# Performance work log

Hardware: AMD Instinct MI355X
Metric: run time of the kernel (lower is better)

The kernel has to match this reference:

```python
import jax, jax.numpy as jnp
import numpy as np

H = 16          # num_heads
D = 1024        # in_features
NH = D // H     # per-head dim
EPS = 1e-5


def _ln(x, g, b):
    m = jnp.mean(x, axis=-1, keepdims=True)
    v = jnp.mean((x - m) ** 2, axis=-1, keepdims=True)
    return (x - m) / jnp.sqrt(v + EPS) * g + b


def _mha(q, k, v, Wq, bq, Wk, bk, Wv, bv, causal):
    # q: [Tq,B,D], k/v: [Tk,B,D]
    Tq, B, _ = q.shape
    Tk = k.shape[0]
    qh = (q @ Wq + bq).reshape(Tq, B, H, NH)
    kh = (k @ Wk + bk).reshape(Tk, B, H, NH)
    vh = (v @ Wv + bv).reshape(Tk, B, H, NH)
    scale = 1.0 / np.float32(np.sqrt(NH))
    logits = jnp.einsum('qbhd,kbhd->bhqk', qh, kh) * scale  # [B,H,Tq,Tk]
    if causal:
        mask = jnp.tril(jnp.ones((Tq, Tk), dtype=bool))
        logits = jnp.where(mask, logits, -jnp.inf)  # softmax over prefix [0..t]
    w = jax.nn.softmax(logits, axis=-1)
    out = jnp.einsum('bhqk,kbhd->qbhd', w, vh).reshape(Tq, B, D)
    return out


def setup_inputs() -> dict:
    key = jax.random.key(0)
    ks = jax.random.split(key, 12)
    s = 0.02
    T, B = 1024, 8
    inp = {
        'encoder_input': jax.random.normal(ks[0], (T, B, D), jnp.float32),
        'decoder_input': jax.random.normal(ks[1], (T, B, D), jnp.float32),
        # self-attention projections
        'Wq1': jax.random.normal(ks[2], (D, D), jnp.float32) * s,
        'bq1': jnp.zeros((D,), jnp.float32),
        'Wk1': jax.random.normal(ks[3], (D, D), jnp.float32) * s,
        'bk1': jnp.zeros((D,), jnp.float32),
        'Wv1': jax.random.normal(ks[4], (D, D), jnp.float32) * s,
        'bv1': jnp.zeros((D,), jnp.float32),
        # cross-attention projections
        'Wq2': jax.random.normal(ks[5], (D, D), jnp.float32) * s,
        'bq2': jnp.zeros((D,), jnp.float32),
        'Wk2': jax.random.normal(ks[6], (D, D), jnp.float32) * s,
        'bk2': jnp.zeros((D,), jnp.float32),
        'Wv2': jax.random.normal(ks[7], (D, D), jnp.float32) * s,
        'bv2': jnp.zeros((D,), jnp.float32),
        # position-wise linear
        'Wl': jax.random.normal(ks[8], (D, D), jnp.float32) * s,
        'bl': jnp.zeros((D,), jnp.float32),
        # layernorms
        'g1': jnp.ones((D,), jnp.float32), 'be1': jnp.zeros((D,), jnp.float32),
        'g2': jnp.ones((D,), jnp.float32), 'be2': jnp.zeros((D,), jnp.float32),
        'g3': jnp.ones((D,), jnp.float32), 'be3': jnp.zeros((D,), jnp.float32),
    }
    return inp


def reference(encoder_input, decoder_input,
              Wq1, bq1, Wk1, bk1, Wv1, bv1,
              Wq2, bq2, Wk2, bk2, Wv2, bv2,
              Wl, bl, g1, be1, g2, be2, g3, be3):
    # causal self-attention (prefix [:t+1] per step == causal mask)
    x = _mha(decoder_input, decoder_input, decoder_input,
             Wq1, bq1, Wk1, bk1, Wv1, bv1, causal=True)
    x = _ln(x + decoder_input, g1, be1)
    # cross-attention over full encoder input
    y = _mha(x, encoder_input, encoder_input,
             Wq2, bq2, Wk2, bk2, Wv2, bv2, causal=False)
    y = _ln(y + x, g2, be2)
    # position-wise linear (no activation in source) + residual + LN
    z = y @ Wl + bl
    out = _ln(z + y, g3, be3)
    return out
```

## Files before the change

kernel.cpp:

```cpp
#include <hip/hip_runtime.h>
#include <hip/hip_bf16.h>

typedef __bf16 bf16x8 __attribute__((ext_vector_type(8)));
typedef float f32x4 __attribute__((ext_vector_type(4)));

#define MFMA16(A, B, C) __builtin_amdgcn_mfma_f32_16x16x32_bf16(A, B, C, 0, 0, 0)

#define GLDS(gp, lp)                                                              \
    __builtin_amdgcn_global_load_lds(                                             \
        (const __attribute__((address_space(1))) void*)(gp),                      \
        (__attribute__((address_space(3))) void*)(lp), 16, 0, 0)

struct PtrW { const float* p[7]; };
__global__ __launch_bounds__(256) void wt_transpose(PtrW W, __hip_bfloat16* __restrict__ Wt) {
    const float* __restrict__ src = W.p[blockIdx.z];
    __hip_bfloat16* __restrict__ dst = Wt + ((size_t)blockIdx.z << 20);
    __shared__ float tile[32][33];
    const int bn = blockIdx.x * 32;
    const int bk = blockIdx.y * 32;
    const int tx = threadIdx.x, ty = threadIdx.y;
#pragma unroll
    for (int i = 0; i < 4; i++) {
        tile[ty + i * 8][tx] = src[(size_t)(bk + ty + i * 8) * 1024 + bn + tx];
    }
    __syncthreads();
#pragma unroll
    for (int i = 0; i < 4; i++) {
        dst[(size_t)(bn + ty + i * 8) * 1024 + bk + tx] =
            __float2bfloat16(tile[tx][ty + i * 8]);
    }
}

struct PtrC { const float* s[2]; __hip_bfloat16* d[2]; };
__global__ __launch_bounds__(256) void to_bf16(PtrC c) {
    const int z = blockIdx.y;
    const int i = (blockIdx.x * 256 + threadIdx.x) * 4;
    const float4 v = *(const float4*)(c.s[z] + i);
    __align__(8) __hip_bfloat16 t[4] = {__float2bfloat16(v.x), __float2bfloat16(v.y),
                                        __float2bfloat16(v.z), __float2bfloat16(v.w)};
    *(uint2*)(c.d[z] + i) = *(const uint2*)t;
}

struct Ptr5 { const float* p[5]; };
__global__ __launch_bounds__(256) void bias_concat(Ptr5 srcs, float* __restrict__ dst) {
    const int i = threadIdx.x * 4;
    *(float4*)(dst + blockIdx.x * 1024 + i) = *(const float4*)(srcs.p[blockIdx.x] + i);
}

__global__ __launch_bounds__(256) void v_transpose(const __hip_bfloat16* __restrict__ src,
                                                   __hip_bfloat16* __restrict__ Vt,
                                                   int S, int coloff) {
    __shared__ __hip_bfloat16 tile[64][72];
    const int t0 = blockIdx.x * 64;
    const int bh = blockIdx.y;
    const int b = bh & 7, h = bh >> 3;
    const int tid = threadIdx.x;
    const int r = tid >> 2, c = (tid & 3) * 16;
    const __hip_bfloat16* sp =
        src + (size_t)((t0 + r) * 8 + b) * S + coloff + h * 64 + c;
    *(uint4*)(&tile[r][c]) = *(const uint4*)(sp);
    *(uint4*)(&tile[r][c + 8]) = *(const uint4*)(sp + 8);
    __syncthreads();
    const int d = tid >> 2, tc = (tid & 3) * 16;
    __align__(16) __hip_bfloat16 tmp[16];
#pragma unroll
    for (int j = 0; j < 16; j++) tmp[j] = tile[tc + j][d];
    __hip_bfloat16* op = Vt + ((size_t)(b * 16 + h) << 16) + (size_t)d * 1024 + t0 + tc;
    *(uint4*)(op) = *(const uint4*)(tmp);
    *(uint4*)(op + 8) = *(const uint4*)(tmp + 8);
}

__global__ __launch_bounds__(256) void gemm_bias_kernel(
    const __hip_bfloat16* __restrict__ A, const __hip_bfloat16* __restrict__ Bt,
    const float* __restrict__ bias, float* __restrict__ Cf,
    __hip_bfloat16* __restrict__ Cb, int M, int N, int K) {
    __shared__ __align__(16) __hip_bfloat16 As[128 * 64];
    __shared__ __align__(16) __hip_bfloat16 Bs[128 * 64];
    const int tid = threadIdx.x;
    const int wave = tid >> 6, lane = tid & 63;
    const int quad = lane >> 4, l16 = lane & 15;
    const int m0 = blockIdx.x * 128, n0 = blockIdx.y * 128;
    const int wm = (wave & 1) * 64, wn = (wave >> 1) * 64;
    const int lrow = lane >> 3;
    const int lch = (lane & 7) ^ (lrow & 7);
    const int sw = l16 & 7;
    const __hip_bfloat16* ap[4];
    const __hip_bfloat16* bp[4];
    __hip_bfloat16* al[4];
    __hip_bfloat16* bl[4];
#pragma unroll
    for (int u = 0; u < 4; u++) {
        const int q = wave * 4 + u;
        const int row = q * 8 + lrow;
        ap[u] = A + (size_t)(m0 + row) * K + lch * 8;
        bp[u] = Bt + (size_t)(n0 + row) * K + lch * 8;
        al[u] = &As[q * 512];
        bl[u] = &Bs[q * 512];
    }
    f32x4 acc[4][4] = {};
    for (int k0 = 0; k0 < K; k0 += 64) {
#pragma unroll
        for (int u = 0; u < 4; u++) {
            GLDS(ap[u] + k0, al[u]);
            GLDS(bp[u] + k0, bl[u]);
        }
        __syncthreads();
        bf16x8 af[2][4], bfr[2][4];
#pragma unroll
        for (int h2 = 0; h2 < 2; h2++)
#pragma unroll
            for (int i = 0; i < 4; i++) {
                af[h2][i] = *(const bf16x8*)(&As[(wm + i * 16 + l16) * 64 +
                                                 (((h2 * 4 + quad) ^ sw) << 3)]);
                bfr[h2][i] = *(const bf16x8*)(&Bs[(wn + i * 16 + l16) * 64 +
                                                  (((h2 * 4 + quad) ^ sw) << 3)]);
            }
        __syncthreads();
#pragma unroll
        for (int h2 = 0; h2 < 2; h2++)
#pragma unroll
            for (int i = 0; i < 4; i++)
#pragma unroll
                for (int j = 0; j < 4; j++)
                    acc[i][j] = MFMA16(af[h2][i], bfr[h2][j], acc[i][j]);
    }
#pragma unroll
    for (int i = 0; i < 4; i++) {
#pragma unroll
        for (int j = 0; j < 4; j++) {
            const int mr = m0 + wm + i * 16 + quad * 4;
            const int nc = n0 + wn + j * 16 + l16;
            const float bv = bias[nc];
#pragma unroll
            for (int r = 0; r < 4; r++) {
                const float v = acc[i][j][r] + bv;
                const size_t idx = (size_t)(mr + r) * N + nc;
                if (Cf) Cf[idx] = v;
                if (Cb) Cb[idx] = __float2bfloat16(v);
            }
        }
    }
}

__global__ __launch_bounds__(256) void attn_kernel(
    const __hip_bfloat16* __restrict__ Qp, const __hip_bfloat16* __restrict__ Kp,
    const __hip_bfloat16* __restrict__ Vt, __hip_bfloat16* __restrict__ Ob,
    int T, int qRS, int kRS, int causal) {
    __shared__ __align__(16) __hip_bfloat16 Ks[64 * 64];
    __shared__ __align__(16) __hip_bfloat16 Vs[64 * 64];
    __shared__ __align__(16) __hip_bfloat16 Ps[4][16 * 64];
    const int tid = threadIdx.x, wave = tid >> 6, lane = tid & 63;
    const int quad = lane >> 4, l16 = lane & 15;
    const int bh = blockIdx.y, b = bh & 7, h = bh >> 3;
    const int q0 = blockIdx.x * 64;
    const int qstride = 8 * qRS, kstride = 8 * kRS;
    const int sw = l16 & 7;
    const float SCL = 0.18033688f;

    const int myq = q0 + wave * 16 + l16;
    bf16x8 qf0, qf1;
    {
        const __hip_bfloat16* qptr = Qp + (size_t)b * qRS + h * 64 + (size_t)myq * qstride;
        qf0 = *(const bf16x8*)(qptr + quad * 8);
        qf1 = *(const bf16x8*)(qptr + 32 + quad * 8);
    }
    const int jk = wave * 2;
    const int lrow = lane >> 3;
    const int lch = (lane & 7) ^ (lrow & 7);
    const __hip_bfloat16* kp0 =
        Kp + (size_t)b * kRS + h * 64 + (size_t)(jk * 8 + lrow) * kstride + lch * 8;
    const __hip_bfloat16* kp1 = kp0 + (size_t)8 * kstride;
    const __hip_bfloat16* vp0 =
        Vt + ((size_t)(b * 16 + h) << 16) + (size_t)(jk * 8 + lrow) * 1024 + lch * 8;
    const __hip_bfloat16* vp1 = vp0 + 8 * 1024;
    __hip_bfloat16* kl0 = &Ks[jk * 512];
    __hip_bfloat16* kl1 = &Ks[jk * 512 + 512];
    __hip_bfloat16* vl0 = &Vs[jk * 512];
    __hip_bfloat16* vl1 = &Vs[jk * 512 + 512];

    float m_i = -1e30f, l_i = 0.f;
    f32x4 o[4] = {};
    const int kend = causal ? (q0 + 64) : T;
    for (int k0 = 0; k0 < kend; k0 += 64) {
        __syncthreads();
        GLDS(kp0 + (size_t)k0 * kstride, kl0);
        GLDS(kp1 + (size_t)k0 * kstride, kl1);
        GLDS(vp0 + k0, vl0);
        GLDS(vp1 + k0, vl1);
        __syncthreads();
        f32x4 s[4];
#pragma unroll
        for (int n = 0; n < 4; n++) {
            f32x4 z = {};
            const int row = (n * 16 + l16) * 64;
            const bf16x8 kf0 = *(const bf16x8*)(&Ks[row + ((quad ^ sw) << 3)]);
            const bf16x8 kf1 = *(const bf16x8*)(&Ks[row + (((quad + 4) ^ sw) << 3)]);
            z = MFMA16(kf0, qf0, z);
            z = MFMA16(kf1, qf1, z);
            s[n] = z;
        }
        const bool nm = causal && (k0 + 63 > q0 + wave * 16);
        float mx = -1e30f;
#pragma unroll
        for (int n = 0; n < 4; n++) {
#pragma unroll
            for (int r = 0; r < 4; r++) {
                float sv = s[n][r] * SCL;
                if (nm && (k0 + n * 16 + quad * 4 + r > myq)) sv = -1e30f;
                s[n][r] = sv;
                mx = fmaxf(mx, sv);
            }
        }
        mx = fmaxf(mx, __shfl_xor(mx, 16));
        mx = fmaxf(mx, __shfl_xor(mx, 32));
        const float mnew = fmaxf(m_i, mx);
        const float alpha = exp2f(m_i - mnew);
        m_i = mnew;
        float sum = 0.f;
#pragma unroll
        for (int n = 0; n < 4; n++) {
            __align__(8) __hip_bfloat16 pb[4];
#pragma unroll
            for (int r = 0; r < 4; r++) {
                const float pv = exp2f(s[n][r] - m_i);
                sum += pv;
                pb[r] = __float2bfloat16(pv);
            }
            const int gcp = 2 * n + (quad >> 1);
            *(uint2*)(&Ps[wave][l16 * 64 + ((gcp ^ sw) << 3) + (quad & 1) * 4]) =
                *(const uint2*)pb;
        }
        sum += __shfl_xor(sum, 16);
        sum += __shfl_xor(sum, 32);
        l_i = l_i * alpha + sum;
#pragma unroll
        for (int mm = 0; mm < 4; mm++) o[mm] = o[mm] * alpha;
        const bf16x8 pf0 = *(const bf16x8*)(&Ps[wave][l16 * 64 + ((quad ^ sw) << 3)]);
        const bf16x8 pf1 =
            *(const bf16x8*)(&Ps[wave][l16 * 64 + (((quad + 4) ^ sw) << 3)]);
#pragma unroll
        for (int mm = 0; mm < 4; mm++) {
            const int vrow = (mm * 16 + l16) * 64;
            const bf16x8 vf0 = *(const bf16x8*)(&Vs[vrow + ((quad ^ sw) << 3)]);
            const bf16x8 vf1 = *(const bf16x8*)(&Vs[vrow + (((quad + 4) ^ sw) << 3)]);
            o[mm] = MFMA16(vf0, pf0, o[mm]);
            o[mm] = MFMA16(vf1, pf1, o[mm]);
        }
    }
    const float inv = 1.0f / l_i;
    __hip_bfloat16* ob = Ob + (size_t)b * 1024 + h * 64 + (size_t)myq * 8192;
#pragma unroll
    for (int mm = 0; mm < 4; mm++) {
        __align__(8) __hip_bfloat16 t[4] = {
            __float2bfloat16(o[mm][0] * inv), __float2bfloat16(o[mm][1] * inv),
            __float2bfloat16(o[mm][2] * inv), __float2bfloat16(o[mm][3] * inv)};
        *(uint2*)(ob + mm * 16 + quad * 4) = *(const uint2*)t;
    }
}

__global__ __launch_bounds__(256) void ln_res_kernel(
    const __hip_bfloat16* __restrict__ a, const float* __restrict__ bres,
    const float* __restrict__ g, const float* __restrict__ be,
    float* __restrict__ outf, __hip_bfloat16* __restrict__ outb) {
    const int row = blockIdx.x;
    const int tid = threadIdx.x;
    const size_t off = (size_t)row * 1024 + tid * 4;
    uint2 ar = *(const uint2*)(a + off);
    const __hip_bfloat16* ah = (const __hip_bfloat16*)&ar;
    const float4 vb = *(const float4*)(bres + off);
    float x0 = __bfloat162float(ah[0]) + vb.x;
    float x1 = __bfloat162float(ah[1]) + vb.y;
    float x2 = __bfloat162float(ah[2]) + vb.z;
    float x3 = __bfloat162float(ah[3]) + vb.w;
    float s = x0 + x1 + x2 + x3;
    float ss = x0 * x0 + x1 * x1 + x2 * x2 + x3 * x3;
#pragma unroll
    for (int w = 32; w >= 1; w >>= 1) {
        s += __shfl_xor(s, w);
        ss += __shfl_xor(ss, w);
    }
    __shared__ float sm[4], sv[4];
    const int wave = tid >> 6;
    if ((tid & 63) == 0) { sm[wave] = s; sv[wave] = ss; }
    __syncthreads();
    s = sm[0] + sm[1] + sm[2] + sm[3];
    ss = sv[0] + sv[1] + sv[2] + sv[3];
    const float mean = s * (1.f / 1024.f);
    const float inv = rsqrtf(ss * (1.f / 1024.f) - mean * mean + 1e-5f);
    const float4 gg = *(const float4*)(g + tid * 4);
    const float4 bb = *(const float4*)(be + tid * 4);
    const float y0 = (x0 - mean) * inv * gg.x + bb.x;
    const float y1 = (x1 - mean) * inv * gg.y + bb.y;
    const float y2 = (x2 - mean) * inv * gg.z + bb.z;
    const float y3 = (x3 - mean) * inv * gg.w + bb.w;
    if (outf) *(float4*)(outf + off) = make_float4(y0, y1, y2, y3);
    if (outb) {
        __align__(8) __hip_bfloat16 t[4] = {__float2bfloat16(y0), __float2bfloat16(y1),
                                            __float2bfloat16(y2), __float2bfloat16(y3)};
        *(uint2*)(outb + off) = *(const uint2*)t;
    }
}

extern "C" void kernel_launch(void* const* d_in, const int* in_sizes, int n_in,
                              void* d_out, int out_size, void* d_ws, size_t ws_size,
                              hipStream_t stream) {
    const float* enc = (const float*)d_in[0];
    const float* dec = (const float*)d_in[1];
    const float* Wq1 = (const float*)d_in[2];
    const float* bq1 = (const float*)d_in[3];
    const float* Wk1 = (const float*)d_in[4];
    const float* bk1 = (const float*)d_in[5];
    const float* Wv1 = (const float*)d_in[6];
    const float* bv1 = (const float*)d_in[7];
    const float* Wq2 = (const float*)d_in[8];
    const float* bq2 = (const float*)d_in[9];
    const float* Wk2 = (const float*)d_in[10];
    const float* bk2 = (const float*)d_in[11];
    const float* Wv2 = (const float*)d_in[12];
    const float* bv2 = (const float*)d_in[13];
    const float* Wl = (const float*)d_in[14];
    const float* bl = (const float*)d_in[15];
    const float* g1 = (const float*)d_in[16];
    const float* be1 = (const float*)d_in[17];
    const float* g2 = (const float*)d_in[18];
    const float* be2 = (const float*)d_in[19];
    const float* g3 = (const float*)d_in[20];
    const float* be3 = (const float*)d_in[21];
    float* outp = (float*)d_out;

    char* p = (char*)d_ws;
    auto alloc = [&](size_t n) {
        char* r = p;
        p += (n + 255) & ~(size_t)255;
        return r;
    };
    const size_t MD = (size_t)8192 * 1024;
    __hip_bfloat16* enc_b = (__hip_bfloat16*)alloc(MD * 2);
    __hip_bfloat16* dec_b = (__hip_bfloat16*)alloc(MD * 2);
    __hip_bfloat16* Wt = (__hip_bfloat16*)alloc((size_t)7 * 1024 * 1024 * 2);
    float* bcat = (float*)alloc((3072 + 2048) * sizeof(float));
    __hip_bfloat16* qkv = (__hip_bfloat16*)alloc(MD * 3 * 2);
    __hip_bfloat16* qb = (__hip_bfloat16*)alloc(MD * 2);
    __hip_bfloat16* attnb = (__hip_bfloat16*)alloc(MD * 2);
    __hip_bfloat16* Vtb = (__hip_bfloat16*)alloc(MD * 2);
    float* xf = (float*)alloc(MD * 4);
    float* yf = (float*)alloc(MD * 4);
    __hip_bfloat16* xb = dec_b;
    __hip_bfloat16* yb = enc_b;

    PtrW wptrs = {{Wq1, Wk1, Wv1, Wq2, Wk2, Wv2, Wl}};
    wt_transpose<<<dim3(32, 32, 7), dim3(32, 8), 0, stream>>>(wptrs, Wt);
    PtrC cp = {{enc, dec}, {enc_b, dec_b}};
    to_bf16<<<dim3(8192, 2), 256, 0, stream>>>(cp);
    Ptr5 bp = {{bq1, bk1, bv1, bk2, bv2}};
    bias_concat<<<5, 256, 0, stream>>>(bp, bcat);

    gemm_bias_kernel<<<dim3(64, 24), 256, 0, stream>>>(dec_b, Wt, bcat, nullptr, qkv,
                                                       8192, 3072, 1024);
    v_transpose<<<dim3(16, 128), 256, 0, stream>>>(qkv, Vtb, 3072, 2048);
    attn_kernel<<<dim3(16, 128), 256, 0, stream>>>(qkv, qkv + 1024, Vtb, attnb,
                                                   1024, 3072, 3072, 1);
    ln_res_kernel<<<8192, 256, 0, stream>>>(attnb, dec, g1, be1, xf, xb);

    gemm_bias_kernel<<<dim3(64, 8), 256, 0, stream>>>(
        xb, Wt + (size_t)3 * 1024 * 1024, bq2, nullptr, qb, 8192, 1024, 1024);
    gemm_bias_kernel<<<dim3(64, 16), 256, 0, stream>>>(
        enc_b, Wt + (size_t)4 * 1024 * 1024, bcat + 3072, nullptr, qkv, 8192, 2048, 1024);
    v_transpose<<<dim3(16, 128), 256, 0, stream>>>(qkv, Vtb, 2048, 1024);
    attn_kernel<<<dim3(16, 128), 256, 0, stream>>>(qb, qkv, Vtb, attnb,
                                                   1024, 1024, 2048, 0);
    ln_res_kernel<<<8192, 256, 0, stream>>>(attnb, xf, g2, be2, yf, yb);

    gemm_bias_kernel<<<dim3(64, 8), 256, 0, stream>>>(
        yb, Wt + (size_t)6 * 1024 * 1024, bl, nullptr, qb, 8192, 1024, 1024);
    ln_res_kernel<<<8192, 256, 0, stream>>>(qb, yf, g3, be3, outp, nullptr);
}
```

Measured before the change: 576.7 us.

## Double-buffer GEMM and attention loads, fold softmax scale into Q projection

```diff
diff --git a/kernel.cpp b/kernel.cpp
--- a/kernel.cpp
+++ b/kernel.cpp
@@ -73,56 +73,57 @@
 __global__ __launch_bounds__(256) void gemm_bias_kernel(
     const __hip_bfloat16* __restrict__ A, const __hip_bfloat16* __restrict__ Bt,
     const float* __restrict__ bias, float* __restrict__ Cf,
-    __hip_bfloat16* __restrict__ Cb, int M, int N, int K) {
-    __shared__ __align__(16) __hip_bfloat16 As[128 * 64];
-    __shared__ __align__(16) __hip_bfloat16 Bs[128 * 64];
+    __hip_bfloat16* __restrict__ Cb, int M, int N, int K,
+    float qscale, int qcols) {
+    __shared__ __align__(16) __hip_bfloat16 As[2][128 * 32];
+    __shared__ __align__(16) __hip_bfloat16 Bs[2][128 * 32];
     const int tid = threadIdx.x;
     const int wave = tid >> 6, lane = tid & 63;
     const int quad = lane >> 4, l16 = lane & 15;
     const int m0 = blockIdx.x * 128, n0 = blockIdx.y * 128;
     const int wm = (wave & 1) * 64, wn = (wave >> 1) * 64;
-    const int lrow = lane >> 3;
-    const int lch = (lane & 7) ^ (lrow & 7);
-    const int sw = l16 & 7;
-    const __hip_bfloat16* ap[4];
-    const __hip_bfloat16* bp[4];
-    __hip_bfloat16* al[4];
-    __hip_bfloat16* bl[4];
-#pragma unroll
-    for (int u = 0; u < 4; u++) {
-        const int q = wave * 4 + u;
-        const int row = q * 8 + lrow;
-        ap[u] = A + (size_t)(m0 + row) * K + lch * 8;
-        bp[u] = Bt + (size_t)(n0 + row) * K + lch * 8;
-        al[u] = &As[q * 512];
-        bl[u] = &Bs[q * 512];
-    }
+    const int srow = lane >> 2;
+    const int lc = (lane & 3) ^ ((lane >> 3) & 3);
+    const __hip_bfloat16* ap[2];
+    const __hip_bfloat16* bp[2];
+    int loff[2];
+#pragma unroll
+    for (int u = 0; u < 2; u++) {
+        const int g = wave * 2 + u;
+        const int row = g * 16 + srow;
+        ap[u] = A + (size_t)(m0 + row) * K + lc * 8;
+        bp[u] = Bt + (size_t)(n0 + row) * K + lc * 8;
+        loff[u] = g * 512;
+    }
+    const int pch = quad ^ ((l16 >> 1) & 3);
     f32x4 acc[4][4] = {};
-    for (int k0 = 0; k0 < K; k0 += 64) {
-#pragma unroll
-        for (int u = 0; u < 4; u++) {
-            GLDS(ap[u] + k0, al[u]);
-            GLDS(bp[u] + k0, bl[u]);
+#pragma unroll
+    for (int u = 0; u < 2; u++) {
+        GLDS(ap[u], &As[0][loff[u]]);
+        GLDS(bp[u], &Bs[0][loff[u]]);
+    }
+    int sel = 0;
+    for (int k0 = 0; k0 < K; k0 += 32) {
+        __syncthreads();
+        if (k0 + 32 < K) {
+#pragma unroll
+            for (int u = 0; u < 2; u++) {
+                GLDS(ap[u] + k0 + 32, &As[sel ^ 1][loff[u]]);
+                GLDS(bp[u] + k0 + 32, &Bs[sel ^ 1][loff[u]]);
+            }
         }
-        __syncthreads();
-        bf16x8 af[2][4], bfr[2][4];
-#pragma unroll
-        for (int h2 = 0; h2 < 2; h2++)
-#pragma unroll
-            for (int i = 0; i < 4; i++) {
-                af[h2][i] = *(const bf16x8*)(&As[(wm + i * 16 + l16) * 64 +
-                                                 (((h2 * 4 + quad) ^ sw) << 3)]);
-                bfr[h2][i] = *(const bf16x8*)(&Bs[(wn + i * 16 + l16) * 64 +
-                                                  (((h2 * 4 + quad) ^ sw) << 3)]);
-            }
-        __syncthreads();
-#pragma unroll
-        for (int h2 = 0; h2 < 2; h2++)
-#pragma unroll
-            for (int i = 0; i < 4; i++)
-#pragma unroll
-                for (int j = 0; j < 4; j++)
-                    acc[i][j] = MFMA16(af[h2][i], bfr[h2][j], acc[i][j]);
+        bf16x8 af[4], bfr[4];
+#pragma unroll
+        for (int i = 0; i < 4; i++) {
+            af[i] = *(const bf16x8*)(&As[sel][(wm + i * 16 + l16) * 32 + pch * 8]);
+            bfr[i] = *(const bf16x8*)(&Bs[sel][(wn + i * 16 + l16) * 32 + pch * 8]);
+        }
+#pragma unroll
+        for (int i = 0; i < 4; i++)
+#pragma unroll
+            for (int j = 0; j < 4; j++)
+                acc[i][j] = MFMA16(af[i], bfr[j], acc[i][j]);
+        sel ^= 1;
     }
 #pragma unroll
     for (int i = 0; i < 4; i++) {
@@ -130,10 +131,11 @@
         for (int j = 0; j < 4; j++) {
             const int mr = m0 + wm + i * 16 + quad * 4;
             const int nc = n0 + wn + j * 16 + l16;
+            const float sc = (nc < qcols) ? qscale : 1.0f;
             const float bv = bias[nc];
 #pragma unroll
             for (int r = 0; r < 4; r++) {
-                const float v = acc[i][j][r] + bv;
+                const float v = (acc[i][j][r] + bv) * sc;
                 const size_t idx = (size_t)(mr + r) * N + nc;
                 if (Cf) Cf[idx] = v;
                 if (Cb) Cb[idx] = __float2bfloat16(v);
@@ -146,16 +148,18 @@
     const __hip_bfloat16* __restrict__ Qp, const __hip_bfloat16* __restrict__ Kp,
     const __hip_bfloat16* __restrict__ Vt, __hip_bfloat16* __restrict__ Ob,
     int T, int qRS, int kRS, int causal) {
-    __shared__ __align__(16) __hip_bfloat16 Ks[64 * 64];
-    __shared__ __align__(16) __hip_bfloat16 Vs[64 * 64];
+    __shared__ __align__(16) __hip_bfloat16 Ks[2][64 * 64];
+    __shared__ __align__(16) __hip_bfloat16 Vs[2][64 * 64];
     __shared__ __align__(16) __hip_bfloat16 Ps[4][16 * 64];
     const int tid = threadIdx.x, wave = tid >> 6, lane = tid & 63;
     const int quad = lane >> 4, l16 = lane & 15;
-    const int bh = blockIdx.y, b = bh & 7, h = bh >> 3;
-    const int q0 = blockIdx.x * 64;
+    const int gid = blockIdx.x;
+    const int bh = (gid & 7) * 16 + (gid >> 7);
+    const int qt = (gid >> 3) & 15;
+    const int b = bh & 7, h = bh >> 3;
+    const int q0 = qt * 64;
     const int qstride = 8 * qRS, kstride = 8 * kRS;
     const int sw = l16 & 7;
-    const float SCL = 0.18033688f;
 
     const int myq = q0 + wave * 16 + l16;
     bf16x8 qf0, qf1;
@@ -164,6 +168,10 @@
         qf0 = *(const bf16x8*)(qptr + quad * 8);
         qf1 = *(const bf16x8*)(qptr + 32 + quad * 8);
     }
+    bf16x8 onesf;
+#pragma unroll
+    for (int i = 0; i < 8; i++) onesf[i] = (__bf16)1.0f;
+
     const int jk = wave * 2;
     const int lrow = lane >> 3;
     const int lch = (lane & 7) ^ (lrow & 7);
@@ -173,81 +181,101 @@
     const __hip_bfloat16* vp0 =
         Vt + ((size_t)(b * 16 + h) << 16) + (size_t)(jk * 8 + lrow) * 1024 + lch * 8;
     const __hip_bfloat16* vp1 = vp0 + 8 * 1024;
-    __hip_bfloat16* kl0 = &Ks[jk * 512];
-    __hip_bfloat16* kl1 = &Ks[jk * 512 + 512];
-    __hip_bfloat16* vl0 = &Vs[jk * 512];
-    __hip_bfloat16* vl1 = &Vs[jk * 512 + 512];
-
-    float m_i = -1e30f, l_i = 0.f;
+    const size_t kinc = (size_t)64 * kstride;
+
+    float m_i = -1e30f;
     f32x4 o[4] = {};
+    f32x4 ol = {};
     const int kend = causal ? (q0 + 64) : T;
+    const int qmax_w = q0 + wave * 16 + 15;
+
+    GLDS(kp0, &Ks[0][jk * 512]);
+    GLDS(kp1, &Ks[0][jk * 512 + 512]);
+    GLDS(vp0, &Vs[0][jk * 512]);
+    GLDS(vp1, &Vs[0][jk * 512 + 512]);
+    const __hip_bfloat16* kn0 = kp0 + kinc;
+    const __hip_bfloat16* kn1 = kp1 + kinc;
+    const __hip_bfloat16* vn0 = vp0 + 64;
+    const __hip_bfloat16* vn1 = vp1 + 64;
+    int sel = 0;
     for (int k0 = 0; k0 < kend; k0 += 64) {
         __syncthreads();
-        GLDS(kp0 + (size_t)k0 * kstride, kl0);
-        GLDS(kp1 + (size_t)k0 * kstride, kl1);
-        GLDS(vp0 + k0, vl0);
-        GLDS(vp1 + k0, vl1);
-        __syncthreads();
-        f32x4 s[4];
-#pragma unroll
-        for (int n = 0; n < 4; n++) {
-            f32x4 z = {};
-            const int row = (n * 16 + l16) * 64;
-            const bf16x8 kf0 = *(const bf16x8*)(&Ks[row + ((quad ^ sw) << 3)]);
-            const bf16x8 kf1 = *(const bf16x8*)(&Ks[row + (((quad + 4) ^ sw) << 3)]);
-            z = MFMA16(kf0, qf0, z);
-            z = MFMA16(kf1, qf1, z);
-            s[n] = z;
+        if (k0 + 64 < kend) {
+            GLDS(kn0, &Ks[sel ^ 1][jk * 512]);
+            GLDS(kn1, &Ks[sel ^ 1][jk * 512 + 512]);
+            GLDS(vn0, &Vs[sel ^ 1][jk * 512]);
+            GLDS(vn1, &Vs[sel ^ 1][jk * 512 + 512]);
+            kn0 += kinc; kn1 += kinc; vn0 += 64; vn1 += 64;
         }
-        const bool nm = causal && (k0 + 63 > q0 + wave * 16);
-        float mx = -1e30f;
-#pragma unroll
-        for (int n = 0; n < 4; n++) {
-#pragma unroll
-            for (int r = 0; r < 4; r++) {
-                float sv = s[n][r] * SCL;
-                if (nm && (k0 + n * 16 + quad * 4 + r > myq)) sv = -1e30f;
-                s[n][r] = sv;
-                mx = fmaxf(mx, sv);
-            }
+        if (!causal || k0 <= qmax_w) {
+            f32x4 s[4];
+#pragma unroll
+            for (int n = 0; n < 4; n++) {
+                f32x4 z = {};
+                const int row = (n * 16 + l16) * 64;
+                const bf16x8 kf0 = *(const bf16x8*)(&Ks[sel][row + ((quad ^ sw) << 3)]);
+                const bf16x8 kf1 =
+                    *(const bf16x8*)(&Ks[sel][row + (((quad + 4) ^ sw) << 3)]);
+                z = MFMA16(kf0, qf0, z);
+                z = MFMA16(kf1, qf1, z);
+                s[n] = z;
+            }
+            const bool nm = causal && (k0 + 63 > q0 + wave * 16);
+            float mx = -1e30f;
+            if (nm) {
+#pragma unroll
+                for (int n = 0; n < 4; n++)
+#pragma unroll
+                    for (int r = 0; r < 4; r++) {
+                        if (k0 + n * 16 + quad * 4 + r > myq) s[n][r] = -1e30f;
+                        mx = fmaxf(mx, s[n][r]);
+                    }
+            } else {
+#pragma unroll
+                for (int n = 0; n < 4; n++)
+#pragma unroll
+                    for (int r = 0; r < 4; r++) mx = fmaxf(mx, s[n][r]);
+            }
+            mx = fmaxf(mx, __shfl_xor(mx, 16));
+            mx = fmaxf(mx, __shfl_xor(mx, 32));
+            const float mnew = fmaxf(m_i, mx);
+            const float alpha = exp2f(m_i - mnew);
+            m_i = mnew;
+#pragma unroll
+            for (int n = 0; n < 4; n++) {
+                const float p0 = exp2f(s[n][0] - m_i);
+                const float p1 = exp2f(s[n][1] - m_i);
+                const float p2 = exp2f(s[n][2] - m_i);
+                const float p3 = exp2f(s[n][3] - m_i);
+                const __hip_bfloat162 pa = __float22bfloat162_rn(make_float2(p0, p1));
+                const __hip_bfloat162 pb = __float22bfloat162_rn(make_float2(p2, p3));
+                uint2 w;
+                w.x = *(const unsigned int*)&pa;
+                w.y = *(const unsigned int*)&pb;
+                const int gcp = 2 * n + (quad >> 1);
+                *(uint2*)(&Ps[wave][l16 * 64 + ((gcp ^ sw) << 3) + (quad & 1) * 4]) = w;
+            }
+#pragma unroll
+            for (int mm = 0; mm < 4; mm++) o[mm] = o[mm] * alpha;
+            ol = ol * alpha;
+            const bf16x8 pf0 = *(const bf16x8*)(&Ps[wave][l16 * 64 + ((quad ^ sw) << 3)]);
+            const bf16x8 pf1 =
+                *(const bf16x8*)(&Ps[wave][l16 * 64 + (((quad + 4) ^ sw) << 3)]);
+#pragma unroll
+            for (int mm = 0; mm < 4; mm++) {
+                const int vrow = (mm * 16 + l16) * 64;
+                const bf16x8 vf0 = *(const bf16x8*)(&Vs[sel][vrow + ((quad ^ sw) << 3)]);
+                const bf16x8 vf1 =
+                    *(const bf16x8*)(&Vs[sel][vrow + (((quad + 4) ^ sw) << 3)]);
+                o[mm] = MFMA16(vf0, pf0, o[mm]);
+                o[mm] = MFMA16(vf1, pf1, o[mm]);
+            }
+            ol = MFMA16(onesf, pf0, ol);
+            ol = MFMA16(onesf, pf1, ol);
         }
-        mx = fmaxf(mx, __shfl_xor(mx, 16));
-        mx = fmaxf(mx, __shfl_xor(mx, 32));
-        const float mnew = fmaxf(m_i, mx);
-        const float alpha = exp2f(m_i - mnew);
-        m_i = mnew;
-        float sum = 0.f;
-#pragma unroll
-        for (int n = 0; n < 4; n++) {
-            __align__(8) __hip_bfloat16 pb[4];
-#pragma unroll
-            for (int r = 0; r < 4; r++) {
-                const float pv = exp2f(s[n][r] - m_i);
-                sum += pv;
-                pb[r] = __float2bfloat16(pv);
-            }
-            const int gcp = 2 * n + (quad >> 1);
-            *(uint2*)(&Ps[wave][l16 * 64 + ((gcp ^ sw) << 3) + (quad & 1) * 4]) =
-                *(const uint2*)pb;
-        }
-        sum += __shfl_xor(sum, 16);
-        sum += __shfl_xor(sum, 32);
-        l_i = l_i * alpha + sum;
-#pragma unroll
-        for (int mm = 0; mm < 4; mm++) o[mm] = o[mm] * alpha;
-        const bf16x8 pf0 = *(const bf16x8*)(&Ps[wave][l16 * 64 + ((quad ^ sw) << 3)]);
-        const bf16x8 pf1 =
-            *(const bf16x8*)(&Ps[wave][l16 * 64 + (((quad + 4) ^ sw) << 3)]);
-#pragma unroll
-        for (int mm = 0; mm < 4; mm++) {
-            const int vrow = (mm * 16 + l16) * 64;
-            const bf16x8 vf0 = *(const bf16x8*)(&Vs[vrow + ((quad ^ sw) << 3)]);
-            const bf16x8 vf1 = *(const bf16x8*)(&Vs[vrow + (((quad + 4) ^ sw) << 3)]);
-            o[mm] = MFMA16(vf0, pf0, o[mm]);
-            o[mm] = MFMA16(vf1, pf1, o[mm]);
-        }
-    }
-    const float inv = 1.0f / l_i;
+        sel ^= 1;
+    }
+    const float inv = 1.0f / ol[0];
     __hip_bfloat16* ob = Ob + (size_t)b * 1024 + h * 64 + (size_t)myq * 8192;
 #pragma unroll
     for (int mm = 0; mm < 4; mm++) {
@@ -348,6 +376,8 @@
     __hip_bfloat16* xb = dec_b;
     __hip_bfloat16* yb = enc_b;
 
+    const float QSC = 0.18033688f;
+
     PtrW wptrs = {{Wq1, Wk1, Wv1, Wq2, Wk2, Wv2, Wl}};
     wt_transpose<<<dim3(32, 32, 7), dim3(32, 8), 0, stream>>>(wptrs, Wt);
     PtrC cp = {{enc, dec}, {enc_b, dec_b}};
@@ -356,22 +386,22 @@
     bias_concat<<<5, 256, 0, stream>>>(bp, bcat);
 
     gemm_bias_kernel<<<dim3(64, 24), 256, 0, stream>>>(dec_b, Wt, bcat, nullptr, qkv,
-                                                       8192, 3072, 1024);
+                                                       8192, 3072, 1024, QSC, 1024);
     v_transpose<<<dim3(16, 128), 256, 0, stream>>>(qkv, Vtb, 3072, 2048);
-    attn_kernel<<<dim3(16, 128), 256, 0, stream>>>(qkv, qkv + 1024, Vtb, attnb,
-                                                   1024, 3072, 3072, 1);
+    attn_kernel<<<2048, 256, 0, stream>>>(qkv, qkv + 1024, Vtb, attnb,
+                                          1024, 3072, 3072, 1);
     ln_res_kernel<<<8192, 256, 0, stream>>>(attnb, dec, g1, be1, xf, xb);
 
     gemm_bias_kernel<<<dim3(64, 8), 256, 0, stream>>>(
-        xb, Wt + (size_t)3 * 1024 * 1024, bq2, nullptr, qb, 8192, 1024, 1024);
+        xb, Wt + (size_t)3 * 1024 * 1024, bq2, nullptr, qb, 8192, 1024, 1024, QSC, 1024);
     gemm_bias_kernel<<<dim3(64, 16), 256, 0, stream>>>(
-        enc_b, Wt + (size_t)4 * 1024 * 1024, bcat + 3072, nullptr, qkv, 8192, 2048, 1024);
+        enc_b, Wt + (size_t)4 * 1024 * 1024, bcat + 3072, nullptr, qkv, 8192, 2048, 1024,
+        1.0f, 0);
     v_transpose<<<dim3(16, 128), 256, 0, stream>>>(qkv, Vtb, 2048, 1024);
-    attn_kernel<<<dim3(16, 128), 256, 0, stream>>>(qb, qkv, Vtb, attnb,
-                                                   1024, 1024, 2048, 0);
+    attn_kernel<<<2048, 256, 0, stream>>>(qb, qkv, Vtb, attnb, 1024, 1024, 2048, 0);
     ln_res_kernel<<<8192, 256, 0, stream>>>(attnb, xf, g2, be2, yf, yb);
 
     gemm_bias_kernel<<<dim3(64, 8), 256, 0, stream>>>(
-        yb, Wt + (size_t)6 * 1024 * 1024, bl, nullptr, qb, 8192, 1024, 1024);
+        yb, Wt + (size_t)6 * 1024 * 1024, bl, nullptr, qb, 8192, 1024, 1024, 1.0f, 0);
     ln_res_kernel<<<8192, 256, 0, stream>>>(qb, yf, g3, be3, outp, nullptr);
 }
```

After: 543.3 us. 1.06x faster.
